# Kernel tuning notes

Measured on AMD Instinct MI355X. Metric: run time of the kernel, lower is better.

The kernel has to match this reference:

```python
import jax, jax.numpy as jnp
import numpy as np

B, IN_DIM, OUT_DIM, NUM_FN = 256, 65536, 65536, 16  # fan_in=2 -> 16 logic functions


def setup_inputs() -> dict:
    key = jax.random.key(0)
    k1, k2, k3 = jax.random.split(key, 3)
    x = jax.random.uniform(k1, (B, IN_DIM), dtype=jnp.float32)
    weights = jax.random.normal(k2, (OUT_DIM, NUM_FN), dtype=jnp.float32)
    # each output neuron picks fan_in=2 input wires
    indices = jax.random.randint(k3, (2, OUT_DIM), 0, IN_DIM, dtype=jnp.int64)
    return {"x": x, "weights": weights, "indices": indices}


def _logic_ops(a, b):
    """All 16 real-valued relaxations of binary boolean functions. [B,OUT,16]."""
    ab = a * b
    one = jnp.ones_like(a)
    zero = jnp.zeros_like(a)
    return jnp.stack([
        zero,                # 0: false
        ab,                  # 1: a AND b
        a - ab,              # 2: a AND NOT b
        a,                   # 3: a
        b - ab,              # 4: NOT a AND b
        b,                   # 5: b
        a + b - 2 * ab,      # 6: a XOR b
        a + b - ab,          # 7: a OR b
        1 - (a + b - ab),    # 8: NOR
        1 - (a + b - 2*ab),  # 9: XNOR
        1 - b,               # 10: NOT b
        1 - b + ab,          # 11: a OR NOT b
        1 - a,               # 12: NOT a
        1 - a + ab,          # 13: NOT a OR b
        1 - ab,              # 14: NAND
        one,                 # 15: true
    ], axis=-1)


def reference(x, weights, indices):
    # gather fan-in inputs: a, b each [B, OUT_DIM]
    a = x[..., indices[0]]
    b = x[..., indices[1]]
    probs = jax.nn.softmax(weights, axis=-1)        # [OUT_DIM, 16] (training path)
    ops = _logic_ops(a, b)                          # [B, OUT_DIM, 16]
    return jnp.einsum('bof,of->bo', ops, probs)     # softmax-weighted combo
```

## Files before the change

kernel.cpp:

```cpp
#include <hip/hip_runtime.h>

#define IN_DIM  65536
#define OUT_DIM 65536
#define BATCH   256


__device__ __forceinline__ float bf2f(unsigned short h) {
    return __uint_as_float(((unsigned int)h) << 16);
}
__device__ __forceinline__ unsigned short f2bf(float f) {
    unsigned int u = __float_as_uint(f);
    u += 0x7FFFu + ((u >> 16) & 1u);
    return (unsigned short)(u >> 16);
}

__device__ __forceinline__ float4 collapse16(const float* w) {
    float m = w[0];
    #pragma unroll
    for (int f = 1; f < 16; ++f) m = fmaxf(m, w[f]);
    float e[16]; float sum = 0.f;
    #pragma unroll
    for (int f = 0; f < 16; ++f) { e[f] = __expf(w[f] - m); sum += e[f]; }
    float inv = 1.0f / sum;
    float w0 = e[8] + e[9] + e[10] + e[11] + e[12] + e[13] + e[14] + e[15];
    float w1 = (e[2] + e[3] + e[6] + e[7]) - (e[8] + e[9] + e[12] + e[13]);
    float w2 = (e[4] + e[5] + e[6] + e[7]) - (e[8] + e[9] + e[10] + e[11]);
    float w3 = e[1] - e[2] - e[4] - 2.f*e[6] - e[7]
             + e[8] + 2.f*e[9] + e[11] + e[13] - e[14];
    return make_float4(w0 * inv, w1 * inv, w2 * inv, w3 * inv);
}

#define TRANS_BLOCKS ((IN_DIM / 64) * (BATCH / 64))
#define COEFF_BLOCKS (OUT_DIM / 256)
#define PAD 69

__global__ __launch_bounds__(256) void prep_kernel(
    const void* __restrict__ x_raw,
    const void* __restrict__ w_raw,
    unsigned int* __restrict__ x_Tb,
    float4* __restrict__ coeffs,
    int trans_blocks)
{
    __shared__ float tile[64][PAD];
    __shared__ int sflag;
    int t  = threadIdx.x;
    int bx = blockIdx.x;

    if (bx < trans_blocks) {
        if (t == 0) sflag = 0;
        __syncthreads();
        if (((const unsigned short*)x_raw)[t] >= 0x3F80u) atomicOr(&sflag, 1);
        __syncthreads();
        int x_is_f32 = sflag;

        int c0 = (bx >> 2) * 64;
        int b0 = (bx & 3) * 64;
        int cq = t & 15;
        int r  = t >> 4;

        if (x_is_f32) {
            const float4* x4 = (const float4*)x_raw;
            #pragma unroll
            for (int k = 0; k < 4; ++k) {
                int row = r + 16 * k;
                float4 v = x4[(size_t)(b0 + row) * (IN_DIM / 4) + (c0 >> 2) + cq];
                tile[row][4 * cq + 0] = v.x;
                tile[row][4 * cq + 1] = v.y;
                tile[row][4 * cq + 2] = v.z;
                tile[row][4 * cq + 3] = v.w;
            }
        } else {
            const uint2* x2 = (const uint2*)x_raw;
            #pragma unroll
            for (int k = 0; k < 4; ++k) {
                int row = r + 16 * k;
                uint2 v = x2[(size_t)(b0 + row) * (IN_DIM / 4) + (c0 >> 2) + cq];
                tile[row][4 * cq + 0] = bf2f((unsigned short)(v.x & 0xFFFFu));
                tile[row][4 * cq + 1] = bf2f((unsigned short)(v.x >> 16));
                tile[row][4 * cq + 2] = bf2f((unsigned short)(v.y & 0xFFFFu));
                tile[row][4 * cq + 3] = bf2f((unsigned short)(v.y >> 16));
            }
        }
        __syncthreads();

        uint4* dst = (uint4*)x_Tb;
        int q   = t & 7;
        int col = t >> 3;
        #pragma unroll
        for (int it = 0; it < 2; ++it) {
            int cc = col + 32 * it;
            unsigned int d[4];
            #pragma unroll
            for (int j = 0; j < 4; ++j) {
                float lo = tile[8 * q + 2 * j][cc];
                float hi = tile[8 * q + 2 * j + 1][cc];
                d[j] = (unsigned int)f2bf(lo) | ((unsigned int)f2bf(hi) << 16);
            }
            dst[(size_t)(c0 + cc) * (BATCH / 8) + (b0 >> 3) + q] =
                make_uint4(d[0], d[1], d[2], d[3]);
        }
    } else {
        if (t == 0) sflag = 0;
        __syncthreads();
        if ((((const unsigned short*)w_raw)[t] & 0x7FFFu) >= 0x4800u) atomicOr(&sflag, 1);
        __syncthreads();
        int w_is_f32 = sflag;

        int o = (bx - trans_blocks) * 256 + t;
        if (o >= OUT_DIM) return;

        float w[16];
        if (w_is_f32) {
            const float4* w4 = reinterpret_cast<const float4*>(w_raw) + (size_t)o * 4;
            float4 q0 = w4[0], q1 = w4[1], q2 = w4[2], q3 = w4[3];
            w[0]=q0.x; w[1]=q0.y; w[2]=q0.z; w[3]=q0.w;
            w[4]=q1.x; w[5]=q1.y; w[6]=q1.z; w[7]=q1.w;
            w[8]=q2.x; w[9]=q2.y; w[10]=q2.z; w[11]=q2.w;
            w[12]=q3.x; w[13]=q3.y; w[14]=q3.z; w[15]=q3.w;
        } else {
            const uint4* w16 = reinterpret_cast<const uint4*>(
                (const unsigned short*)w_raw + (size_t)o * 16);
            uint4 p0 = w16[0], p1 = w16[1];
            unsigned int pk[8] = { p0.x, p0.y, p0.z, p0.w, p1.x, p1.y, p1.z, p1.w };
            #pragma unroll
            for (int i = 0; i < 8; ++i) {
                w[2*i]   = bf2f((unsigned short)(pk[i] & 0xFFFFu));
                w[2*i+1] = bf2f((unsigned short)(pk[i] >> 16));
            }
        }
        coeffs[o] = collapse16(w);
    }
}

__global__ __launch_bounds__(256) void logic_bt_kernel(
    const unsigned int* __restrict__ x_Tb,
    const void* __restrict__ idx_raw,
    const float4* __restrict__ coeffs,
    float* __restrict__ out)
{
    __shared__ uint4 rows4[64 * 32];
    __shared__ int sflag;
    int t = threadIdx.x;
    if (t == 0) sflag = 0;
    __syncthreads();
    if ((t & 1) && ((const int*)idx_raw)[t] != 0) atomicOr(&sflag, 1);
    __syncthreads();
    int idx_is_i32 = sflag;

    int o0 = blockIdx.x * 32;

    int rr = t >> 5;
    int l  = t & 31;
    int wires[8];
    if (idx_is_i32) {
        const int* p = (const int*)idx_raw;
        #pragma unroll
        for (int ps = 0; ps < 8; ++ps) {
            int r = rr + 8 * ps;
            wires[ps] = p[(r >> 5) * OUT_DIM + o0 + (r & 31)];
        }
    } else {
        const long long* p = (const long long*)idx_raw;
        #pragma unroll
        for (int ps = 0; ps < 8; ++ps) {
            int r = rr + 8 * ps;
            wires[ps] = (int)p[(r >> 5) * OUT_DIM + o0 + (r & 31)];
        }
    }

    const uint4* src4 = (const uint4*)x_Tb;
    #pragma unroll
    for (int ps = 0; ps < 8; ++ps) {
        int r = rr + 8 * ps;
        uint4 v = src4[((size_t)wires[ps] << 5) + l];
        rows4[r * 32 + (l ^ (r & 31))] = v;
    }

    float4 c = coeffs[o0 + (t & 31)];
    __syncthreads();

    int o = t & 31;
    const uint4* ra4 = rows4 + o * 32;
    const uint4* rb4 = rows4 + (32 + o) * 32;
    float* outp = out + o0 + o;
    #pragma unroll
    for (int i = 0; i < 4; ++i) {
        int bq = (t >> 5) + 8 * i;
        uint4 ua = ra4[bq ^ o];
        uint4 ub = rb4[bq ^ o];
        unsigned int pa[4] = { ua.x, ua.y, ua.z, ua.w };
        unsigned int pb[4] = { ub.x, ub.y, ub.z, ub.w };
        int base = bq * 8;
        #pragma unroll
        for (int j = 0; j < 4; ++j) {
            float a0 = bf2f((unsigned short)(pa[j] & 0xFFFFu));
            float a1 = bf2f((unsigned short)(pa[j] >> 16));
            float v0 = bf2f((unsigned short)(pb[j] & 0xFFFFu));
            float v1 = bf2f((unsigned short)(pb[j] >> 16));
            float r0v = fmaf(v0, fmaf(c.w, a0, c.z), fmaf(c.y, a0, c.x));
            float r1v = fmaf(v1, fmaf(c.w, a1, c.z), fmaf(c.y, a1, c.x));
            __builtin_nontemporal_store(r0v, outp + (size_t)(base + 2*j)     * OUT_DIM);
            __builtin_nontemporal_store(r1v, outp + (size_t)(base + 2*j + 1) * OUT_DIM);
        }
    }
}

__global__ __launch_bounds__(256) void logic_direct_kernel(
    const void* __restrict__ x_raw,
    const void* __restrict__ idx_raw,
    const float4* __restrict__ coeffs,
    float* __restrict__ out)
{
    __shared__ int sflag;
    int t = threadIdx.x;
    if (t == 0) sflag = 0;
    __syncthreads();
    int fl = 0;
    if (((const unsigned short*)x_raw)[t] >= 0x3F80u) fl |= 1;
    if ((t & 1) && ((const int*)idx_raw)[t] != 0) fl |= 2;
    if (fl) atomicOr(&sflag, fl);
    __syncthreads();
    int x_is_f32   = sflag & 1;
    int idx_is_i32 = (sflag >> 1) & 1;

    int o = blockIdx.x * 256 + t;
    int ia, ib;
    if (idx_is_i32) {
        const int* p = (const int*)idx_raw;
        ia = p[o];       ib = p[OUT_DIM + o];
    } else {
        const long long* p = (const long long*)idx_raw;
        ia = (int)p[o];  ib = (int)p[OUT_DIM + o];
    }
    float4 c = coeffs[o];
    int b0 = blockIdx.y * 32;

    if (x_is_f32) {
        const float* xa = (const float*)x_raw + ia;
        const float* xb = (const float*)x_raw + ib;
        #pragma unroll 8
        for (int r = 0; r < 32; ++r) {
            int b = b0 + r;
            float av = xa[(size_t)b * IN_DIM];
            float bv = xb[(size_t)b * IN_DIM];
            out[(size_t)b * OUT_DIM + o] =
                fmaf(bv, fmaf(c.w, av, c.z), fmaf(c.y, av, c.x));
        }
    } else {
        const unsigned short* xa = (const unsigned short*)x_raw + ia;
        const unsigned short* xb = (const unsigned short*)x_raw + ib;
        #pragma unroll 8
        for (int r = 0; r < 32; ++r) {
            int b = b0 + r;
            float av = bf2f(xa[(size_t)b * IN_DIM]);
            float bv = bf2f(xb[(size_t)b * IN_DIM]);
            out[(size_t)b * OUT_DIM + o] =
                fmaf(bv, fmaf(c.w, av, c.z), fmaf(c.y, av, c.x));
        }
    }
}

extern "C" void kernel_launch(void* const* d_in, const int* in_sizes, int n_in,
                              void* d_out, int out_size, void* d_ws, size_t ws_size,
                              hipStream_t stream) {
    const void* x       = d_in[0];
    const void* weights = d_in[1];
    const void* indices = d_in[2];
    float*      out     = (float*)d_out;

    float4*       coeffs = (float4*)((char*)d_ws + 256);
    unsigned int* x_Tb   = (unsigned int*)((char*)d_ws + 2u * 1024u * 1024u);

    const size_t need = 2u * 1024u * 1024u +
                        (size_t)IN_DIM * (BATCH / 2) * sizeof(unsigned int);

    if (ws_size >= need) {
        prep_kernel<<<dim3(TRANS_BLOCKS + COEFF_BLOCKS), dim3(256), 0, stream>>>(
            x, weights, x_Tb, coeffs, TRANS_BLOCKS);
        logic_bt_kernel<<<dim3(OUT_DIM / 32), dim3(256), 0, stream>>>(
            x_Tb, indices, coeffs, out);
    } else {
        prep_kernel<<<dim3(COEFF_BLOCKS), dim3(256), 0, stream>>>(
            x, weights, x_Tb, coeffs, 0);
        dim3 grid(OUT_DIM / 256, BATCH / 32);
        logic_direct_kernel<<<grid, dim3(256), 0, stream>>>(
            x, indices, coeffs, out);
    }
}
```

Baseline: 139.0 us.

## Fuse prep and logic kernels into one persistent cooperative kernel with grid sync

Replaces the two-kernel sequence (transpose/coefficient prep, then gather-and-evaluate) with a single persistent cooperative kernel. Blocks loop over the coefficient, transpose and logic tiles, separated by a grid-wide barrier, and the shared memory for the two phases is overlaid in a union. The goal is to remove the second launch and the gap between kernels. The cost is a grid sync, a grid capped at 1024 blocks that may lower parallelism in the gather phase, and a fallback to the old path if the cooperative launch fails.

```diff
diff --git a/kernel.cpp b/kernel.cpp
--- a/kernel.cpp
+++ b/kernel.cpp
@@ -1,4 +1,7 @@
 #include <hip/hip_runtime.h>
+#include <hip/hip_cooperative_groups.h>
+
+namespace cg = cooperative_groups;
 
 #define IN_DIM  65536
 #define OUT_DIM 65536
@@ -30,85 +33,48 @@
     return make_float4(w0 * inv, w1 * inv, w2 * inv, w3 * inv);
 }
 
-#define TRANS_BLOCKS ((IN_DIM / 64) * (BATCH / 64))
+#define TRANS_TILES ((IN_DIM / 64) * (BATCH / 64))
+#define LOGIC_TILES (OUT_DIM / 32)
+#define TRANS_BLOCKS TRANS_TILES
 #define COEFF_BLOCKS (OUT_DIM / 256)
 #define PAD 69
 
-__global__ __launch_bounds__(256) void prep_kernel(
+struct __align__(16) LdsU {
+    union {
+        float tile[64][PAD];
+        uint4 rows4[64 * 32];
+    };
+};
+
+__global__ __launch_bounds__(256, 4) void fused_kernel(
     const void* __restrict__ x_raw,
     const void* __restrict__ w_raw,
+    const void* __restrict__ idx_raw,
     unsigned int* __restrict__ x_Tb,
     float4* __restrict__ coeffs,
-    int trans_blocks)
+    float* __restrict__ out)
 {
-    __shared__ float tile[64][PAD];
+    __shared__ LdsU u;
     __shared__ int sflag;
     int t  = threadIdx.x;
     int bx = blockIdx.x;
-
-    if (bx < trans_blocks) {
-        if (t == 0) sflag = 0;
-        __syncthreads();
-        if (((const unsigned short*)x_raw)[t] >= 0x3F80u) atomicOr(&sflag, 1);
-        __syncthreads();
-        int x_is_f32 = sflag;
-
-        int c0 = (bx >> 2) * 64;
-        int b0 = (bx & 3) * 64;
-        int cq = t & 15;
-        int r  = t >> 4;
-
-        if (x_is_f32) {
-            const float4* x4 = (const float4*)x_raw;
-            #pragma unroll
-            for (int k = 0; k < 4; ++k) {
-                int row = r + 16 * k;
-                float4 v = x4[(size_t)(b0 + row) * (IN_DIM / 4) + (c0 >> 2) + cq];
-                tile[row][4 * cq + 0] = v.x;
-                tile[row][4 * cq + 1] = v.y;
-                tile[row][4 * cq + 2] = v.z;
-                tile[row][4 * cq + 3] = v.w;
-            }
-        } else {
-            const uint2* x2 = (const uint2*)x_raw;
-            #pragma unroll
-            for (int k = 0; k < 4; ++k) {
-                int row = r + 16 * k;
-                uint2 v = x2[(size_t)(b0 + row) * (IN_DIM / 4) + (c0 >> 2) + cq];
-                tile[row][4 * cq + 0] = bf2f((unsigned short)(v.x & 0xFFFFu));
-                tile[row][4 * cq + 1] = bf2f((unsigned short)(v.x >> 16));
-                tile[row][4 * cq + 2] = bf2f((unsigned short)(v.y & 0xFFFFu));
-                tile[row][4 * cq + 3] = bf2f((unsigned short)(v.y >> 16));
-            }
-        }
-        __syncthreads();
-
-        uint4* dst = (uint4*)x_Tb;
-        int q   = t & 7;
-        int col = t >> 3;
-        #pragma unroll
-        for (int it = 0; it < 2; ++it) {
-            int cc = col + 32 * it;
-            unsigned int d[4];
-            #pragma unroll
-            for (int j = 0; j < 4; ++j) {
-                float lo = tile[8 * q + 2 * j][cc];
-                float hi = tile[8 * q + 2 * j + 1][cc];
-                d[j] = (unsigned int)f2bf(lo) | ((unsigned int)f2bf(hi) << 16);
-            }
-            dst[(size_t)(c0 + cc) * (BATCH / 8) + (b0 >> 3) + q] =
-                make_uint4(d[0], d[1], d[2], d[3]);
-        }
-    } else {
-        if (t == 0) sflag = 0;
-        __syncthreads();
-        if ((((const unsigned short*)w_raw)[t] & 0x7FFFu) >= 0x4800u) atomicOr(&sflag, 1);
-        __syncthreads();
-        int w_is_f32 = sflag;
-
-        int o = (bx - trans_blocks) * 256 + t;
-        if (o >= OUT_DIM) return;
-
+    int nb = gridDim.x;
+
+    if (t == 0) sflag = 0;
+    __syncthreads();
+    {
+        int fl = 0;
+        if (((const unsigned short*)x_raw)[t] >= 0x3F80u) fl |= 1;
+        if ((((const unsigned short*)w_raw)[t] & 0x7FFFu) >= 0x4800u) fl |= 2;
+        if ((t & 1) && ((const int*)idx_raw)[t] != 0) fl |= 4;
+        if (fl) atomicOr(&sflag, fl);
+    }
+    __syncthreads();
+    const int x_is_f32   = sflag & 1;
+    const int w_is_f32   = (sflag >> 1) & 1;
+    const int idx_is_i32 = (sflag >> 2) & 1;
+
+    for (int o = bx * 256 + t; o < OUT_DIM; o += nb * 256) {
         float w[16];
         if (w_is_f32) {
             const float4* w4 = reinterpret_cast<const float4*>(w_raw) + (size_t)o * 4;
@@ -130,6 +96,216 @@
         }
         coeffs[o] = collapse16(w);
     }
+
+    for (int tid = bx; tid < TRANS_TILES; tid += nb) {
+        int c0 = (tid >> 2) * 64;
+        int b0 = (tid & 3) * 64;
+        int cq = t & 15;
+        int r  = t >> 4;
+
+        __syncthreads();
+        if (x_is_f32) {
+            const float4* x4 = (const float4*)x_raw;
+            #pragma unroll
+            for (int k = 0; k < 4; ++k) {
+                int row = r + 16 * k;
+                float4 v = x4[(size_t)(b0 + row) * (IN_DIM / 4) + (c0 >> 2) + cq];
+                u.tile[row][4 * cq + 0] = v.x;
+                u.tile[row][4 * cq + 1] = v.y;
+                u.tile[row][4 * cq + 2] = v.z;
+                u.tile[row][4 * cq + 3] = v.w;
+            }
+        } else {
+            const uint2* x2 = (const uint2*)x_raw;
+            #pragma unroll
+            for (int k = 0; k < 4; ++k) {
+                int row = r + 16 * k;
+                uint2 v = x2[(size_t)(b0 + row) * (IN_DIM / 4) + (c0 >> 2) + cq];
+                u.tile[row][4 * cq + 0] = bf2f((unsigned short)(v.x & 0xFFFFu));
+                u.tile[row][4 * cq + 1] = bf2f((unsigned short)(v.x >> 16));
+                u.tile[row][4 * cq + 2] = bf2f((unsigned short)(v.y & 0xFFFFu));
+                u.tile[row][4 * cq + 3] = bf2f((unsigned short)(v.y >> 16));
+            }
+        }
+        __syncthreads();
+
+        uint4* dst = (uint4*)x_Tb;
+        int q   = t & 7;
+        int col = t >> 3;
+        #pragma unroll
+        for (int it = 0; it < 2; ++it) {
+            int cc = col + 32 * it;
+            unsigned int d[4];
+            #pragma unroll
+            for (int j = 0; j < 4; ++j) {
+                float lo = u.tile[8 * q + 2 * j][cc];
+                float hi = u.tile[8 * q + 2 * j + 1][cc];
+                d[j] = (unsigned int)f2bf(lo) | ((unsigned int)f2bf(hi) << 16);
+            }
+            dst[(size_t)(c0 + cc) * (BATCH / 8) + (b0 >> 3) + q] =
+                make_uint4(d[0], d[1], d[2], d[3]);
+        }
+    }
+
+    __threadfence();
+    cg::this_grid().sync();
+    __threadfence();
+
+    const uint4* src4 = (const uint4*)x_Tb;
+    for (int lt = bx; lt < LOGIC_TILES; lt += nb) {
+        int o0 = lt * 32;
+        int rr = t >> 5;
+        int l  = t & 31;
+
+        int wires[8];
+        if (idx_is_i32) {
+            const int* p = (const int*)idx_raw;
+            #pragma unroll
+            for (int ps = 0; ps < 8; ++ps) {
+                int r = rr + 8 * ps;
+                wires[ps] = p[(r >> 5) * OUT_DIM + o0 + (r & 31)];
+            }
+        } else {
+            const long long* p = (const long long*)idx_raw;
+            #pragma unroll
+            for (int ps = 0; ps < 8; ++ps) {
+                int r = rr + 8 * ps;
+                wires[ps] = (int)p[(r >> 5) * OUT_DIM + o0 + (r & 31)];
+            }
+        }
+
+        __syncthreads();
+        #pragma unroll
+        for (int ps = 0; ps < 8; ++ps) {
+            int r = rr + 8 * ps;
+            u.rows4[r * 32 + (l ^ (r & 31))] = src4[((size_t)wires[ps] << 5) + l];
+        }
+        float4 c = coeffs[o0 + (t & 31)];
+        __syncthreads();
+
+        int o = t & 31;
+        const uint4* ra4 = u.rows4 + o * 32;
+        const uint4* rb4 = u.rows4 + (32 + o) * 32;
+        float* outp = out + o0 + o;
+        #pragma unroll
+        for (int i = 0; i < 4; ++i) {
+            int bq = (t >> 5) + 8 * i;
+            uint4 ua = ra4[bq ^ o];
+            uint4 ub = rb4[bq ^ o];
+            unsigned int pa[4] = { ua.x, ua.y, ua.z, ua.w };
+            unsigned int pb[4] = { ub.x, ub.y, ub.z, ub.w };
+            int base = bq * 8;
+            #pragma unroll
+            for (int j = 0; j < 4; ++j) {
+                float a0 = bf2f((unsigned short)(pa[j] & 0xFFFFu));
+                float a1 = bf2f((unsigned short)(pa[j] >> 16));
+                float v0 = bf2f((unsigned short)(pb[j] & 0xFFFFu));
+                float v1 = bf2f((unsigned short)(pb[j] >> 16));
+                float r0v = fmaf(v0, fmaf(c.w, a0, c.z), fmaf(c.y, a0, c.x));
+                float r1v = fmaf(v1, fmaf(c.w, a1, c.z), fmaf(c.y, a1, c.x));
+                __builtin_nontemporal_store(r0v, outp + (size_t)(base + 2*j)     * OUT_DIM);
+                __builtin_nontemporal_store(r1v, outp + (size_t)(base + 2*j + 1) * OUT_DIM);
+            }
+        }
+    }
+}
+
+__global__ __launch_bounds__(256) void prep_kernel(
+    const void* __restrict__ x_raw,
+    const void* __restrict__ w_raw,
+    unsigned int* __restrict__ x_Tb,
+    float4* __restrict__ coeffs,
+    int trans_blocks)
+{
+    __shared__ float tile[64][PAD];
+    __shared__ int sflag;
+    int t  = threadIdx.x;
+    int bx = blockIdx.x;
+
+    if (bx < trans_blocks) {
+        if (t == 0) sflag = 0;
+        __syncthreads();
+        if (((const unsigned short*)x_raw)[t] >= 0x3F80u) atomicOr(&sflag, 1);
+        __syncthreads();
+        int x_is_f32 = sflag;
+
+        int c0 = (bx >> 2) * 64;
+        int b0 = (bx & 3) * 64;
+        int cq = t & 15;
+        int r  = t >> 4;
+
+        if (x_is_f32) {
+            const float4* x4 = (const float4*)x_raw;
+            #pragma unroll
+            for (int k = 0; k < 4; ++k) {
+                int row = r + 16 * k;
+                float4 v = x4[(size_t)(b0 + row) * (IN_DIM / 4) + (c0 >> 2) + cq];
+                tile[row][4 * cq + 0] = v.x;
+                tile[row][4 * cq + 1] = v.y;
+                tile[row][4 * cq + 2] = v.z;
+                tile[row][4 * cq + 3] = v.w;
+            }
+        } else {
+            const uint2* x2 = (const uint2*)x_raw;
+            #pragma unroll
+            for (int k = 0; k < 4; ++k) {
+                int row = r + 16 * k;
+                uint2 v = x2[(size_t)(b0 + row) * (IN_DIM / 4) + (c0 >> 2) + cq];
+                tile[row][4 * cq + 0] = bf2f((unsigned short)(v.x & 0xFFFFu));
+                tile[row][4 * cq + 1] = bf2f((unsigned short)(v.x >> 16));
+                tile[row][4 * cq + 2] = bf2f((unsigned short)(v.y & 0xFFFFu));
+                tile[row][4 * cq + 3] = bf2f((unsigned short)(v.y >> 16));
+            }
+        }
+        __syncthreads();
+
+        uint4* dst = (uint4*)x_Tb;
+        int q   = t & 7;
+        int col = t >> 3;
+        #pragma unroll
+        for (int it = 0; it < 2; ++it) {
+            int cc = col + 32 * it;
+            unsigned int d[4];
+            #pragma unroll
+            for (int j = 0; j < 4; ++j) {
+                float lo = tile[8 * q + 2 * j][cc];
+                float hi = tile[8 * q + 2 * j + 1][cc];
+                d[j] = (unsigned int)f2bf(lo) | ((unsigned int)f2bf(hi) << 16);
+            }
+            dst[(size_t)(c0 + cc) * (BATCH / 8) + (b0 >> 3) + q] =
+                make_uint4(d[0], d[1], d[2], d[3]);
+        }
+    } else {
+        if (t == 0) sflag = 0;
+        __syncthreads();
+        if ((((const unsigned short*)w_raw)[t] & 0x7FFFu) >= 0x4800u) atomicOr(&sflag, 1);
+        __syncthreads();
+        int w_is_f32 = sflag;
+
+        int o = (bx - trans_blocks) * 256 + t;
+        if (o >= OUT_DIM) return;
+
+        float w[16];
+        if (w_is_f32) {
+            const float4* w4 = reinterpret_cast<const float4*>(w_raw) + (size_t)o * 4;
+            float4 q0 = w4[0], q1 = w4[1], q2 = w4[2], q3 = w4[3];
+            w[0]=q0.x; w[1]=q0.y; w[2]=q0.z; w[3]=q0.w;
+            w[4]=q1.x; w[5]=q1.y; w[6]=q1.z; w[7]=q1.w;
+            w[8]=q2.x; w[9]=q2.y; w[10]=q2.z; w[11]=q2.w;
+            w[12]=q3.x; w[13]=q3.y; w[14]=q3.z; w[15]=q3.w;
+        } else {
+            const uint4* w16 = reinterpret_cast<const uint4*>(
+                (const unsigned short*)w_raw + (size_t)o * 16);
+            uint4 p0 = w16[0], p1 = w16[1];
+            unsigned int pk[8] = { p0.x, p0.y, p0.z, p0.w, p1.x, p1.y, p1.z, p1.w };
+            #pragma unroll
+            for (int i = 0; i < 8; ++i) {
+                w[2*i]   = bf2f((unsigned short)(pk[i] & 0xFFFFu));
+                w[2*i+1] = bf2f((unsigned short)(pk[i] >> 16));
+            }
+        }
+        coeffs[o] = collapse16(w);
+    }
 }
 
 __global__ __launch_bounds__(256) void logic_bt_kernel(
@@ -148,7 +324,6 @@
     int idx_is_i32 = sflag;
 
     int o0 = blockIdx.x * 32;
-
     int rr = t >> 5;
     int l  = t & 31;
     int wires[8];
@@ -172,10 +347,8 @@
     #pragma unroll
     for (int ps = 0; ps < 8; ++ps) {
         int r = rr + 8 * ps;
-        uint4 v = src4[((size_t)wires[ps] << 5) + l];
-        rows4[r * 32 + (l ^ (r & 31))] = v;
-    }
-
+        rows4[r * 32 + (l ^ (r & 31))] = src4[((size_t)wires[ps] << 5) + l];
+    }
     float4 c = coeffs[o0 + (t & 31)];
     __syncthreads();
 
@@ -275,10 +448,32 @@
                         (size_t)IN_DIM * (BATCH / 2) * sizeof(unsigned int);
 
     if (ws_size >= need) {
-        prep_kernel<<<dim3(TRANS_BLOCKS + COEFF_BLOCKS), dim3(256), 0, stream>>>(
-            x, weights, x_Tb, coeffs, TRANS_BLOCKS);
-        logic_bt_kernel<<<dim3(OUT_DIM / 32), dim3(256), 0, stream>>>(
-            x_Tb, indices, coeffs, out);
+        static int s_nb = 0;
+        if (s_nb == 0) {
+            int maxPerCU = 0;
+            if (hipOccupancyMaxActiveBlocksPerMultiprocessor(
+                    &maxPerCU, reinterpret_cast<const void*>(fused_kernel),
+                    256, 0) != hipSuccess || maxPerCU < 1) {
+                maxPerCU = 2;
+            }
+            long nb = (long)maxPerCU * 256;
+            if (nb > 1024) nb = 1024;
+            s_nb = (int)nb;
+        }
+
+        void* args[] = { (void*)&x, (void*)&weights, (void*)&indices,
+                         (void*)&x_Tb, (void*)&coeffs, (void*)&out };
+        hipError_t err = hipLaunchCooperativeKernel(
+            reinterpret_cast<const void*>(fused_kernel),
+            dim3(s_nb), dim3(256), args, 0, stream);
+
+        if (err != hipSuccess) {
+            (void)hipGetLastError();
+            prep_kernel<<<dim3(TRANS_BLOCKS + COEFF_BLOCKS), dim3(256), 0, stream>>>(
+                x, weights, x_Tb, coeffs, TRANS_BLOCKS);
+            logic_bt_kernel<<<dim3(OUT_DIM / 32), dim3(256), 0, stream>>>(
+                x_Tb, indices, coeffs, out);
+        }
     } else {
         prep_kernel<<<dim3(COEFF_BLOCKS), dim3(256), 0, stream>>>(
             x, weights, x_Tb, coeffs, 0);
```

Result: slower. 383.6 us (+175.9%).
